# Kernel tuning notes

Hardware: AMD Instinct MI355X
Metric: run time of the kernel (lower is better)

The kernel has to match this reference:

```python
import jax, jax.numpy as jnp
import numpy as np
import math

B, A, T = 64, 23, 128          # batch, num_agents, max seq len
D, AE, S, H = 256, 32, 6, 8    # d_model, agent_encoding_dim, static_dim, heads
DK = D // H                     # 32
DM = D + AE                     # 288, MHA q/k/v dim
NEG = -1e10                     # masked_fill constant from source


def sinusoidal_pe(pos, d):
    # pos: int array [...], returns [..., d] standard transformer PE at positions pos
    half = jnp.arange(d // 2, dtype=jnp.float32)
    div = jnp.exp(-half * (math.log(10000.0) * 2.0 / d))          # [d/2]
    ang = pos[..., None].astype(jnp.float32) * div                # [..., d/2]
    return jnp.stack([jnp.sin(ang), jnp.cos(ang)], axis=-1).reshape(*pos.shape, d)


def setup_inputs() -> dict:
    key = jax.random.key(0)
    ks = jax.random.split(key, 20)
    std = 0.02
    data = jax.random.normal(ks[0], (B, A, T), jnp.float32)
    lengths = jax.random.randint(ks[1], (B, A), 0, T + 1).astype(jnp.int32)   # mask arg = lengths
    t = jnp.arange(T, dtype=jnp.int32)
    time = jnp.where(t[None, None, :] < lengths[:, :, None], t[None, None, :], -1)  # [B,A,T], -1 = pad
    static = jax.random.normal(ks[2], (B, S), jnp.float32)
    # per-agent Linear(1, D): weight [A, D], bias [A, D]
    W_embed = std * jax.random.normal(ks[3], (A, D), jnp.float32)
    b_embed = std * jax.random.normal(ks[4], (A, D), jnp.float32)
    E_var = std * jax.random.normal(ks[5], (A, AE), jnp.float32)            # VariateEncoding table
    W_static = std * jax.random.normal(ks[6], (S, D), jnp.float32)
    b_static = jnp.zeros((D,), jnp.float32)
    Wq = std * jax.random.normal(ks[7], (DM, D), jnp.float32); bq = jnp.zeros((D,), jnp.float32)
    Wk = std * jax.random.normal(ks[8], (DM, D), jnp.float32); bk = jnp.zeros((D,), jnp.float32)
    Wv = std * jax.random.normal(ks[9], (DM, D), jnp.float32); bv = jnp.zeros((D,), jnp.float32)
    Wo = std * jax.random.normal(ks[10], (D, DM), jnp.float32); bo = jnp.zeros((DM,), jnp.float32)
    Wg = std * jax.random.normal(ks[11], (DM + D, 1), jnp.float32); bg = jnp.zeros((1,), jnp.float32)
    return dict(data=data, time=time, mask=lengths, static=static,
                W_embed=W_embed, b_embed=b_embed, E_var=E_var,
                W_static=W_static, b_static=b_static,
                Wq=Wq, bq=bq, Wk=Wk, bk=bk, Wv=Wv, bv=bv, Wo=Wo, bo=bo,
                Wg=Wg, bg=bg)


def reference(data, time, mask, static, W_embed, b_embed, E_var, W_static, b_static,
              Wq, bq, Wk, bk, Wv, bv, Wo, bo, Wg, bg):
    lengths = mask                                            # [B,A] sequence lengths
    t = jnp.arange(T)
    valid = t[None, None, :] < lengths[:, :, None]            # [B,A,T] bool
    # mask_matrix[i,:len,:len]=1 double loop -> vectorized outer product
    mask4 = valid[:, :, :, None] & valid[:, :, None, :]       # [B,A,T,T]

    # per-agent Linear(1, D) loop -> batched rank-1 affine, then ReLU
    data_embeds = jax.nn.relu(data[..., None] * W_embed[None, :, None, :]
                              + b_embed[None, :, None, :])    # [B,A,T,D]

    # src_pe: sinusoidal positional encoding at (clamped) time values
    pe = sinusoidal_pe(jnp.maximum(time, 0), D)               # [B,A,T,D]
    src = data_embeds + pe

    # variate (agent-id) embedding concat -> [B,A,T,D+AE]; encoder = identity
    var = jnp.broadcast_to(E_var[None, :, None, :], (B, A, T, AE))
    memory = jnp.concatenate([src, var], axis=-1)             # [B,A,T,DM]

    # time-masked mean pool over T
    time_mask = time >= 0                                     # [B,A,T]
    memory = jnp.where(time_mask[..., None], memory, 0.0)
    counts = time_mask.sum(axis=2).astype(memory.dtype)       # [B,A]
    agentwise = memory.sum(axis=2) / (counts[..., None] + 1e-9)  # [B,A,DM]

    # custom MHA (dim='Time'): q_len = 1 per agent, keys/values over T
    q = jnp.einsum('bae,ed->bad', agentwise, Wq) + bq          # [B,A,D]
    k = jnp.einsum('bate,ed->batd', memory, Wk) + bk           # [B,A,T,D]
    v = jnp.einsum('bate,ed->batd', memory, Wv) + bv
    qh = q.reshape(B, A, H, DK)                                # [B,A,H,DK] (q_len=1 squeezed)
    kh = k.reshape(B, A, T, H, DK).transpose(0, 1, 3, 2, 4)    # [B,A,H,T,DK]
    vh = v.reshape(B, A, T, H, DK).transpose(0, 1, 3, 2, 4)
    scores = jnp.einsum('bahd,bahtd->baht', qh, kh) / math.sqrt(DK)  # [B,A,H,T]
    amask = mask4[:, :, 0, :]                                  # [B,A,T] row 0 of per-agent mask
    scores = jnp.where(amask[:, :, None, :], scores, NEG)
    p = jax.nn.softmax(scores, axis=-1)                        # dropout = eval (identity)
    ctx = jnp.einsum('baht,bahtd->bahd', p, vh).reshape(B, A, D)
    agent_feat = jnp.einsum('bad,de->bae', ctx, Wo) + bo       # [B,A,DM]

    # agent-masked mean pool over agents
    agent_mask = counts > 0                                    # [B,A]
    agent_feat = jnp.where(agent_mask[..., None], agent_feat, 0.0)
    denom = agent_mask.sum(axis=1).astype(agent_feat.dtype) + 1e-9
    aggre = agent_feat.sum(axis=1) / denom[:, None]            # [B,DM]

    static_feat = static @ W_static + b_static                 # [B,D]
    all_feature = jnp.concatenate([aggre, static_feat], axis=-1)  # [B,DM+D]
    return all_feature @ Wg + bg                               # [B,1]


if __name__ == '__main__':
    out = reference(**setup_inputs())
    print(out.shape, jnp.asarray(out).dtype)
```

## Files before the change

### kernel.cpp

```cpp
#include <hip/hip_runtime.h>
#include <math.h>

#define NB 64
#define NA 23
#define NT 128
#define ND 256
#define NAE 32
#define NS 6
#define NH 8
#define NDM 288

#define OFF_PET    0
#define OFF_PECUM  32768
#define OFF_WKT    65792
#define OFF_VWO    131328
#define OFF_CST    133632
#define OFF_S      133648

__global__ __launch_bounds__(256) void setup_kernel(
    const float* __restrict__ Wk, const float* __restrict__ Wv,
    const float* __restrict__ Wo, const float* __restrict__ Wg,
    const float* __restrict__ bv, const float* __restrict__ bo,
    const float* __restrict__ W_static, const float* __restrict__ b_static,
    const float* __restrict__ bg, float* __restrict__ ws)
{
    const int blk = blockIdx.x;
    const int tid = threadIdx.x;
    float* peT   = ws + OFF_PET;
    float* PEcum = ws + OFF_PECUM;
    float* WkT   = ws + OFF_WKT;
    float* VWo   = ws + OFF_VWO;
    float* cst   = ws + OFF_CST;

    if (blk < 128) {
        const int g = tid >> 7, t = tid & 127;
        const int e = blk * 2 + g;
        const int i = e >> 1;
        const float kdiv = 0.07195578415606394f;
        const float dv = expf(-(float)i * kdiv);
        const float ang = (float)t * dv;
        const float v = (e & 1) ? cosf(ang) : sinf(ang);
        peT[e * NT + t] = v;
        __shared__ float buf[256];
        buf[tid] = v;
        #pragma unroll
        for (int s = 1; s < 128; s <<= 1) {
            __syncthreads();
            float add = (t >= s) ? buf[tid - s] : 0.f;
            __syncthreads();
            buf[tid] += add;
        }
        __syncthreads();
        PEcum[(t + 1) * ND + e] = buf[tid];
    } else if (blk < 384) {
        const int j = blk - 128;
        const float scale = 0.17677669529663687f;
        WkT[j * 256 + tid] = Wk[tid * ND + j] * scale;
    } else if (blk < 392) {
        const int h = blk - 384;
        __shared__ float wog[32];
        {
            const int jj = tid >> 3, sub = tid & 7;
            const int j = h * 32 + jj;
            float acc = 0.f;
            const int m0 = sub * 36;
            #pragma unroll 4
            for (int m = m0; m < m0 + 36; ++m)
                acc = fmaf(Wo[j * NDM + m], Wg[m], acc);
            acc += __shfl_down(acc, 4, 8);
            acc += __shfl_down(acc, 2, 8);
            acc += __shfl_down(acc, 1, 8);
            if (sub == 0) wog[jj] = acc;
        }
        __syncthreads();
        for (int e = tid; e < NDM; e += 256) {
            float acc = 0.f;
            #pragma unroll 8
            for (int jj = 0; jj < 32; ++jj)
                acc = fmaf(Wv[e * ND + h * 32 + jj], wog[jj], acc);
            VWo[h * NDM + e] = acc;
        }
        if (tid == 0) {
            float acc = 0.f;
            #pragma unroll 8
            for (int jj = 0; jj < 32; ++jj)
                acc = fmaf(bv[h * 32 + jj], wog[jj], acc);
            cst[8 + h] = acc;
        }
    } else {
        const int i = tid >> 5, sub = tid & 31;
        float acc = 0.f;
        if (i < 6) {
            for (int m = sub; m < 256; m += 32)
                acc = fmaf(W_static[i * ND + m], Wg[NDM + m], acc);
        } else if (i == 6) {
            for (int m = sub; m < 256; m += 32)
                acc = fmaf(b_static[m], Wg[NDM + m], acc);
        } else {
            for (int m = sub; m < NDM; m += 32)
                acc = fmaf(bo[m], Wg[m], acc);
        }
        #pragma unroll
        for (int off = 16; off > 0; off >>= 1)
            acc += __shfl_down(acc, off, 32);
        if (sub == 0) cst[i] = (i == 6) ? acc + bg[0] : acc;
    }
}

__global__ __launch_bounds__(256) void main_kernel(
    const float* __restrict__ data, const int* __restrict__ lengths,
    const float* __restrict__ W_embed, const float* __restrict__ b_embed,
    const float* __restrict__ E_var,
    const float* __restrict__ Wq, const float* __restrict__ bq,
    float* __restrict__ ws)
{
    const int wg = blockIdx.x;
    const int a = wg % NA;
    const int tid = threadIdx.x;
    const int L = lengths[wg];

    if (L == 0) {
        if (tid == 0) ws[OFF_S + wg] = 0.f;
        return;
    }

    __shared__ float xs[NT];
    __shared__ float agentwise[NDM];
    __shared__ float qs[ND];
    __shared__ float2 Wb[ND];
    __shared__ __align__(16) float combo[ND * 20];
    __shared__ float evvS[NH];
    __shared__ float red[4];

    const float* peT   = ws + OFF_PET;
    const float* PEcum = ws + OFF_PECUM;
    const float* WkT   = ws + OFF_WKT;
    const float* VWo   = ws + OFF_VWO;
    const float* cstp  = ws + OFF_CST;

    if (tid < NT) xs[tid] = data[wg * NT + tid];
    __syncthreads();
    {
        const int e = tid;
        const float We = W_embed[a * ND + e];
        const float be = b_embed[a * ND + e];
        Wb[e] = make_float2(We, be);
        float s0 = 0.f, s1 = 0.f, s2 = 0.f, s3 = 0.f;
        int t = 0;
        for (; t + 4 <= L; t += 4) {
            s0 += fmaxf(fmaf(xs[t],     We, be), 0.f);
            s1 += fmaxf(fmaf(xs[t + 1], We, be), 0.f);
            s2 += fmaxf(fmaf(xs[t + 2], We, be), 0.f);
            s3 += fmaxf(fmaf(xs[t + 3], We, be), 0.f);
        }
        for (; t < L; ++t)
            s0 += fmaxf(fmaf(xs[t], We, be), 0.f);
        agentwise[e] = (((s0 + s1) + (s2 + s3)) + PEcum[L * ND + e]) / (float)L;
    }
    if (tid < NAE) agentwise[ND + tid] = E_var[a * NAE + tid];
    __syncthreads();

    {
        const int j = tid;
        float acc = bq[j];
        #pragma unroll 4
        for (int f = 0; f < NDM; ++f)
            acc = fmaf(agentwise[f], Wq[f * ND + j], acc);
        qs[j] = acc;
    }
    __syncthreads();

    {
        const int h = tid >> 5, eo = tid & 31;
        const float* wr = WkT + (h * 32) * 256;
        const float* qh = qs + h * 32;
        for (int eb = 0; eb < 8; ++eb) {
            const int e = eb * 32 + eo;
            float acc = 0.f, acc2 = 0.f;
            #pragma unroll
            for (int j = 0; j < 32; j += 2) {
                acc  = fmaf(wr[ j      * 256 + e], qh[j],     acc);
                acc2 = fmaf(wr[(j + 1) * 256 + e], qh[j + 1], acc2);
            }
            combo[e * 20 + h] = acc + acc2;
        }
    }
    for (int idx = tid; idx < NH * ND; idx += 256) {
        const int h = idx >> 8, e = idx & 255;
        combo[e * 20 + 8 + h] = VWo[h * NDM + e];
    }
    {
        const int h = tid >> 5, ee = tid & 31;
        float v = agentwise[ND + ee] * VWo[h * NDM + ND + ee];
        v += __shfl_down(v, 16, 32);
        v += __shfl_down(v, 8, 32);
        v += __shfl_down(v, 4, 32);
        v += __shfl_down(v, 2, 32);
        v += __shfl_down(v, 1, 32);
        if (ee == 0) evvS[h] = v;
    }
    __syncthreads();

    {
        const int t  = tid & 63;
        const int hh = (tid >> 6) & 1;
        const int c  = tid >> 7;
        const int ebase = c * 128;
        const float xt1 = xs[t];
        const float xt2 = xs[t + 64];
        const float* peCol = peT + ebase * NT + t;
        const float4* comboV = (const float4*)combo;
        float aS1[4], aS2[4], aM1[4], aM2[4];
        #pragma unroll
        for (int k = 0; k < 4; ++k) { aS1[k] = 0.f; aS2[k] = 0.f; aM1[k] = 0.f; aM2[k] = 0.f; }

        if (L > 64) {
            #pragma unroll 2
            for (int ee = 0; ee < 128; ++ee) {
                const int e = ebase + ee;
                const float2 wb = Wb[e];
                const float pe1 = peCol[ee * NT];
                const float pe2 = peCol[ee * NT + 64];
                const float lin1 = fmaf(xt1, wb.x, wb.y);
                const float lin2 = fmaf(xt2, wb.x, wb.y);
                const float m1 = fmaxf(lin1, 0.f) + pe1;
                const float m2 = fmaxf(lin2, 0.f) + pe2;
                const float4 cq = comboV[e * 5 + hh];
                const float4 cm = comboV[e * 5 + 2 + hh];
                aS1[0] = fmaf(m1, cq.x, aS1[0]); aS1[1] = fmaf(m1, cq.y, aS1[1]);
                aS1[2] = fmaf(m1, cq.z, aS1[2]); aS1[3] = fmaf(m1, cq.w, aS1[3]);
                aS2[0] = fmaf(m2, cq.x, aS2[0]); aS2[1] = fmaf(m2, cq.y, aS2[1]);
                aS2[2] = fmaf(m2, cq.z, aS2[2]); aS2[3] = fmaf(m2, cq.w, aS2[3]);
                aM1[0] = fmaf(m1, cm.x, aM1[0]); aM1[1] = fmaf(m1, cm.y, aM1[1]);
                aM1[2] = fmaf(m1, cm.z, aM1[2]); aM1[3] = fmaf(m1, cm.w, aM1[3]);
                aM2[0] = fmaf(m2, cm.x, aM2[0]); aM2[1] = fmaf(m2, cm.y, aM2[1]);
                aM2[2] = fmaf(m2, cm.z, aM2[2]); aM2[3] = fmaf(m2, cm.w, aM2[3]);
            }
        } else {
            #pragma unroll 2
            for (int ee = 0; ee < 128; ++ee) {
                const int e = ebase + ee;
                const float2 wb = Wb[e];
                const float pe1 = peCol[ee * NT];
                const float m1 = fmaxf(fmaf(xt1, wb.x, wb.y), 0.f) + pe1;
                const float4 cq = comboV[e * 5 + hh];
                const float4 cm = comboV[e * 5 + 2 + hh];
                aS1[0] = fmaf(m1, cq.x, aS1[0]); aS1[1] = fmaf(m1, cq.y, aS1[1]);
                aS1[2] = fmaf(m1, cq.z, aS1[2]); aS1[3] = fmaf(m1, cq.w, aS1[3]);
                aM1[0] = fmaf(m1, cm.x, aM1[0]); aM1[1] = fmaf(m1, cm.y, aM1[1]);
                aM1[2] = fmaf(m1, cm.z, aM1[2]); aM1[3] = fmaf(m1, cm.w, aM1[3]);
            }
        }
        __syncthreads();
        float* scF = combo;
        float* mvF = combo + 1024;
        float* pS  = combo + 2048;
        float* pM  = combo + 3072;
        if (c == 1) {
            #pragma unroll
            for (int k = 0; k < 4; ++k) {
                const int h = hh * 4 + k;
                pS[h * NT + t]      = aS1[k];
                pS[h * NT + t + 64] = aS2[k];
                pM[h * NT + t]      = aM1[k];
                pM[h * NT + t + 64] = aM2[k];
            }
        }
        __syncthreads();
        if (c == 0) {
            #pragma unroll
            for (int k = 0; k < 4; ++k) {
                const int h = hh * 4 + k;
                scF[h * NT + t]      = aS1[k] + pS[h * NT + t];
                scF[h * NT + t + 64] = aS2[k] + pS[h * NT + t + 64];
                mvF[h * NT + t]      = aM1[k] + pM[h * NT + t];
                mvF[h * NT + t + 64] = aM2[k] + pM[h * NT + t + 64];
            }
        }
    }
    __syncthreads();

    {
        const float* sc  = combo;
        const float* mvb = combo + 1024;
        const int wv = tid >> 6, lane = tid & 63;
        float wsum = 0.f;
        for (int hh = 0; hh < 2; ++hh) {
            const int h = wv * 2 + hh;
            float s1 = (lane < L) ? sc[h * NT + lane] : -3e38f;
            float s2 = (lane + 64 < L) ? sc[h * NT + 64 + lane] : -3e38f;
            float mx = fmaxf(s1, s2);
            #pragma unroll
            for (int off = 32; off > 0; off >>= 1)
                mx = fmaxf(mx, __shfl_down(mx, off, 64));
            mx = __shfl(mx, 0, 64);
            const float vbv = evvS[h] + cstp[8 + h];
            float e1 = (lane < L) ? __expf(s1 - mx) : 0.f;
            float e2 = (lane + 64 < L) ? __expf(s2 - mx) : 0.f;
            float num = e1 * (mvb[h * NT + lane] + vbv);
            num = fmaf(e2, mvb[h * NT + 64 + lane] + vbv, num);
            float den = e1 + e2;
            #pragma unroll
            for (int off = 32; off > 0; off >>= 1) {
                num += __shfl_down(num, off, 64);
                den += __shfl_down(den, off, 64);
            }
            if (lane == 0) wsum += num / den;
        }
        if (lane == 0) red[wv] = wsum;
    }
    __syncthreads();
    if (tid == 0)
        ws[OFF_S + wg] = cstp[7] + red[0] + red[1] + red[2] + red[3];
}

__global__ __launch_bounds__(64) void final_kernel(
    const float* __restrict__ statics, const int* __restrict__ lengths,
    const float* __restrict__ ws, float* __restrict__ out)
{
    const int b = threadIdx.x;
    const float* s_arr = ws + OFF_S;
    const float* cst = ws + OFF_CST;
    float sum = 0.f;
    int n = 0;
    for (int a = 0; a < NA; ++a) {
        if (lengths[b * NA + a] > 0) { sum += s_arr[b * NA + a]; ++n; }
    }
    float o = sum / ((float)n + 1e-9f);
    #pragma unroll
    for (int i = 0; i < NS; ++i)
        o = fmaf(statics[b * NS + i], cst[i], o);
    o += cst[6];
    out[b] = o;
}

extern "C" void kernel_launch(void* const* d_in, const int* in_sizes, int n_in,
                              void* d_out, int out_size, void* d_ws, size_t ws_size,
                              hipStream_t stream) {
    const float* data     = (const float*)d_in[0];
    const int*   mask     = (const int*)d_in[2];
    const float* statics  = (const float*)d_in[3];
    const float* W_embed  = (const float*)d_in[4];
    const float* b_embed  = (const float*)d_in[5];
    const float* E_var    = (const float*)d_in[6];
    const float* W_static = (const float*)d_in[7];
    const float* b_static = (const float*)d_in[8];
    const float* Wq       = (const float*)d_in[9];
    const float* bq       = (const float*)d_in[10];
    const float* Wk       = (const float*)d_in[11];
    const float* Wv       = (const float*)d_in[13];
    const float* bv       = (const float*)d_in[14];
    const float* Wo       = (const float*)d_in[15];
    const float* bo       = (const float*)d_in[16];
    const float* Wg       = (const float*)d_in[17];
    const float* bg       = (const float*)d_in[18];
    float* out = (float*)d_out;
    float* ws  = (float*)d_ws;

    setup_kernel<<<dim3(393), dim3(256), 0, stream>>>(Wk, Wv, Wo, Wg, bv, bo,
                                                      W_static, b_static, bg, ws);
    main_kernel<<<dim3(NB * NA), dim3(256), 0, stream>>>(data, mask, W_embed, b_embed,
                                                         E_var, Wq, bq, ws);
    final_kernel<<<dim3(1), dim3(64), 0, stream>>>(statics, mask, ws, out);
}
```

Before: 174.4 us.

## Precompute positional-encoding key/value projections and restructure per-agent attention

Splits the positional-encoding contribution out of the per-timestep score and value terms. A new setup kernel precomputes PE·Wk and PE·VWo once per timestep, so the main kernel's inner loop no longer streams a PE column from global memory. The Q projection becomes float4-vectorised across four partial sums, the combo table shrinks to an XOR-swizzled 16-float row, and E_var·V terms are precomputed per agent. Per-agent results are accumulated into per-batch slots with atomics, which adds an extra kernel launch and makes the summation order nondeterministic.

```diff
diff --git a/kernel.cpp b/kernel.cpp
--- a/kernel.cpp
+++ b/kernel.cpp
@@ -10,23 +10,25 @@
 #define NH 8
 #define NDM 288
 
-#define OFF_PET    0
+#define OFF_PEK    0
 #define OFF_PECUM  32768
-#define OFF_WKT    65792
-#define OFF_VWO    131328
-#define OFF_CST    133632
-#define OFF_S      133648
-
-__global__ __launch_bounds__(256) void setup_kernel(
+#define OFF_WKT    65536
+#define OFF_VWO    131072
+#define OFF_PEMV   133120
+#define OFF_EVA    134144
+#define OFF_CST    134328
+#define OFF_SB     134336
+
+__global__ __launch_bounds__(256) void setup1_kernel(
     const float* __restrict__ Wk, const float* __restrict__ Wv,
     const float* __restrict__ Wo, const float* __restrict__ Wg,
     const float* __restrict__ bv, const float* __restrict__ bo,
     const float* __restrict__ W_static, const float* __restrict__ b_static,
-    const float* __restrict__ bg, float* __restrict__ ws)
+    const float* __restrict__ bg, const float* __restrict__ E_var,
+    float* __restrict__ ws)
 {
     const int blk = blockIdx.x;
     const int tid = threadIdx.x;
-    float* peT   = ws + OFF_PET;
     float* PEcum = ws + OFF_PECUM;
     float* WkT   = ws + OFF_WKT;
     float* VWo   = ws + OFF_VWO;
@@ -40,7 +42,6 @@
         const float dv = expf(-(float)i * kdiv);
         const float ang = (float)t * dv;
         const float v = (e & 1) ? cosf(ang) : sinf(ang);
-        peT[e * NT + t] = v;
         __shared__ float buf[256];
         buf[tid] = v;
         #pragma unroll
@@ -51,7 +52,7 @@
             buf[tid] += add;
         }
         __syncthreads();
-        PEcum[(t + 1) * ND + e] = buf[tid];
+        PEcum[t * ND + e] = buf[tid];
     } else if (blk < 384) {
         const int j = blk - 128;
         const float scale = 0.17677669529663687f;
@@ -59,6 +60,8 @@
     } else if (blk < 392) {
         const int h = blk - 384;
         __shared__ float wog[32];
+        __shared__ float vext[32];
+        __shared__ float vbS;
         {
             const int jj = tid >> 3, sub = tid & 7;
             const int j = h * 32 + jj;
@@ -73,19 +76,34 @@
             if (sub == 0) wog[jj] = acc;
         }
         __syncthreads();
-        for (int e = tid; e < NDM; e += 256) {
+        {
             float acc = 0.f;
             #pragma unroll 8
             for (int jj = 0; jj < 32; ++jj)
-                acc = fmaf(Wv[e * ND + h * 32 + jj], wog[jj], acc);
-            VWo[h * NDM + e] = acc;
+                acc = fmaf(Wv[tid * ND + h * 32 + jj], wog[jj], acc);
+            VWo[h * 256 + tid] = acc;
+        }
+        if (tid < 32) {
+            float acc = 0.f;
+            #pragma unroll 8
+            for (int jj = 0; jj < 32; ++jj)
+                acc = fmaf(Wv[(256 + tid) * ND + h * 32 + jj], wog[jj], acc);
+            vext[tid] = acc;
         }
         if (tid == 0) {
             float acc = 0.f;
             #pragma unroll 8
             for (int jj = 0; jj < 32; ++jj)
                 acc = fmaf(bv[h * 32 + jj], wog[jj], acc);
-            cst[8 + h] = acc;
+            vbS = acc;
+        }
+        __syncthreads();
+        if (tid < NA) {
+            float acc = vbS;
+            #pragma unroll 8
+            for (int ee = 0; ee < 32; ++ee)
+                acc = fmaf(E_var[tid * NAE + ee], vext[ee], acc);
+            ws[OFF_EVA + tid * NH + h] = acc;
         }
     } else {
         const int i = tid >> 5, sub = tid & 31;
@@ -107,6 +125,49 @@
     }
 }
 
+__global__ __launch_bounds__(256) void setup2_kernel(
+    const float* __restrict__ Wk, float* __restrict__ ws)
+{
+    const int t = blockIdx.x;
+    const int tid = threadIdx.x;
+    __shared__ float peS[256];
+    {
+        const int i = tid >> 1;
+        const float kdiv = 0.07195578415606394f;
+        const float dv = expf(-(float)i * kdiv);
+        const float ang = (float)t * dv;
+        peS[tid] = (tid & 1) ? cosf(ang) : sinf(ang);
+    }
+    __syncthreads();
+    {
+        float a0 = 0.f, a1 = 0.f, a2 = 0.f, a3 = 0.f;
+        #pragma unroll 4
+        for (int e = 0; e < 256; e += 4) {
+            a0 = fmaf(peS[e],     Wk[ e      * ND + tid], a0);
+            a1 = fmaf(peS[e + 1], Wk[(e + 1) * ND + tid], a1);
+            a2 = fmaf(peS[e + 2], Wk[(e + 2) * ND + tid], a2);
+            a3 = fmaf(peS[e + 3], Wk[(e + 3) * ND + tid], a3);
+        }
+        const float scale = 0.17677669529663687f;
+        ws[OFF_PEK + t * 256 + tid] = ((a0 + a1) + (a2 + a3)) * scale;
+    }
+    {
+        const int h = tid >> 5, ee = tid & 31;
+        const float* vw = ws + OFF_VWO + h * 256;
+        float v = 0.f;
+        #pragma unroll
+        for (int k = 0; k < 8; ++k)
+            v = fmaf(peS[ee + 32 * k], vw[ee + 32 * k], v);
+        v += __shfl_down(v, 16, 32);
+        v += __shfl_down(v, 8, 32);
+        v += __shfl_down(v, 4, 32);
+        v += __shfl_down(v, 2, 32);
+        v += __shfl_down(v, 1, 32);
+        if (ee == 0) ws[OFF_PEMV + h * NT + t] = v;
+    }
+    if (t == 0 && tid < NB) ws[OFF_SB + tid] = 0.f;
+}
+
 __global__ __launch_bounds__(256) void main_kernel(
     const float* __restrict__ data, const int* __restrict__ lengths,
     const float* __restrict__ W_embed, const float* __restrict__ b_embed,
@@ -116,23 +177,20 @@
 {
     const int wg = blockIdx.x;
     const int a = wg % NA;
+    const int b = wg / NA;
     const int tid = threadIdx.x;
     const int L = lengths[wg];
 
-    if (L == 0) {
-        if (tid == 0) ws[OFF_S + wg] = 0.f;
-        return;
-    }
+    if (L == 0) return;
 
     __shared__ float xs[NT];
     __shared__ float agentwise[NDM];
-    __shared__ float qs[ND];
+    __shared__ __align__(16) float qs[ND];
     __shared__ float2 Wb[ND];
-    __shared__ __align__(16) float combo[ND * 20];
-    __shared__ float evvS[NH];
+    __shared__ __align__(16) float combo[ND * 16];
+    __shared__ __align__(16) float qkx[NH * NT];
     __shared__ float red[4];
 
-    const float* peT   = ws + OFF_PET;
     const float* PEcum = ws + OFF_PECUM;
     const float* WkT   = ws + OFF_WKT;
     const float* VWo   = ws + OFF_VWO;
@@ -155,49 +213,78 @@
         }
         for (; t < L; ++t)
             s0 += fmaxf(fmaf(xs[t], We, be), 0.f);
-        agentwise[e] = (((s0 + s1) + (s2 + s3)) + PEcum[L * ND + e]) / (float)L;
+        agentwise[e] = (((s0 + s1) + (s2 + s3)) + PEcum[(L - 1) * ND + e]) / (float)L;
     }
     if (tid < NAE) agentwise[ND + tid] = E_var[a * NAE + tid];
     __syncthreads();
 
     {
-        const int j = tid;
-        float acc = bq[j];
+        const int lane = tid & 63;
+        const int fc = tid >> 6;
+        const float4* Wq4 = (const float4*)Wq;
+        float a0 = 0.f, a1 = 0.f, a2 = 0.f, a3 = 0.f;
+        const int f0 = fc * 72;
         #pragma unroll 4
-        for (int f = 0; f < NDM; ++f)
-            acc = fmaf(agentwise[f], Wq[f * ND + j], acc);
-        qs[j] = acc;
-    }
-    __syncthreads();
-
-    {
-        const int h = tid >> 5, eo = tid & 31;
-        const float* wr = WkT + (h * 32) * 256;
-        const float* qh = qs + h * 32;
-        for (int eb = 0; eb < 8; ++eb) {
-            const int e = eb * 32 + eo;
-            float acc = 0.f, acc2 = 0.f;
+        for (int f = f0; f < f0 + 72; ++f) {
+            const float ag = agentwise[f];
+            const float4 w = Wq4[f * 64 + lane];
+            a0 = fmaf(ag, w.x, a0);
+            a1 = fmaf(ag, w.y, a1);
+            a2 = fmaf(ag, w.z, a2);
+            a3 = fmaf(ag, w.w, a3);
+        }
+        ((float4*)qkx)[fc * 64 + lane] = make_float4(a0, a1, a2, a3);
+    }
+    __syncthreads();
+    qs[tid] = bq[tid] + qkx[tid] + qkx[256 + tid] + qkx[512 + tid] + qkx[768 + tid];
+    __syncthreads();
+
+    {
+        const int e = tid;
+        const float* wcol = WkT + e;
+        const int r = e & 3;
+        float4* row = (float4*)combo + e * 4;
+        float qk[8];
+        #pragma unroll
+        for (int h = 0; h < 8; ++h) {
+            const float* wr = wcol + (h * 32) * 256;
+            const float* qh = qs + h * 32;
+            float c0 = 0.f, c1 = 0.f;
             #pragma unroll
             for (int j = 0; j < 32; j += 2) {
-                acc  = fmaf(wr[ j      * 256 + e], qh[j],     acc);
-                acc2 = fmaf(wr[(j + 1) * 256 + e], qh[j + 1], acc2);
-            }
-            combo[e * 20 + h] = acc + acc2;
-        }
-    }
-    for (int idx = tid; idx < NH * ND; idx += 256) {
-        const int h = idx >> 8, e = idx & 255;
-        combo[e * 20 + 8 + h] = VWo[h * NDM + e];
-    }
-    {
-        const int h = tid >> 5, ee = tid & 31;
-        float v = agentwise[ND + ee] * VWo[h * NDM + ND + ee];
-        v += __shfl_down(v, 16, 32);
-        v += __shfl_down(v, 8, 32);
-        v += __shfl_down(v, 4, 32);
-        v += __shfl_down(v, 2, 32);
-        v += __shfl_down(v, 1, 32);
-        if (ee == 0) evvS[h] = v;
+                c0 = fmaf(wr[ j      * 256], qh[j],     c0);
+                c1 = fmaf(wr[(j + 1) * 256], qh[j + 1], c1);
+            }
+            qk[h] = c0 + c1;
+        }
+        row[0 ^ r] = make_float4(qk[0], qk[1], qk[2], qk[3]);
+        row[1 ^ r] = make_float4(qk[4], qk[5], qk[6], qk[7]);
+        row[2 ^ r] = make_float4(VWo[0 * 256 + e], VWo[1 * 256 + e],
+                                 VWo[2 * 256 + e], VWo[3 * 256 + e]);
+        row[3 ^ r] = make_float4(VWo[4 * 256 + e], VWo[5 * 256 + e],
+                                 VWo[6 * 256 + e], VWo[7 * 256 + e]);
+    }
+    __syncthreads();
+    {
+        const int h = tid >> 5, t0 = tid & 31;
+        const float4* qs4  = (const float4*)qs;
+        const float4* PEK4 = (const float4*)(ws + OFF_PEK);
+        #pragma unroll
+        for (int tt = 0; tt < 4; ++tt) {
+            const int t = t0 + tt * 32;
+            const float4* pk = PEK4 + t * 64 + h * 8;
+            float b0 = 0.f, b1 = 0.f, b2 = 0.f, b3 = 0.f;
+            #pragma unroll
+            for (int jq = 0; jq < 8; ++jq) {
+                const float4 q = qs4[h * 8 + jq];
+                const float4 p = pk[jq];
+                b0 = fmaf(q.x, p.x, b0);
+                b1 = fmaf(q.y, p.y, b1);
+                b2 = fmaf(q.z, p.z, b2);
+                b3 = fmaf(q.w, p.w, b3);
+            }
+            qkx[h * NT + t] = (b0 + b1) + (b2 + b3);
+        }
     }
     __syncthreads();
 
@@ -208,25 +295,21 @@
         const int ebase = c * 128;
         const float xt1 = xs[t];
         const float xt2 = xs[t + 64];
-        const float* peCol = peT + ebase * NT + t;
         const float4* comboV = (const float4*)combo;
         float aS1[4], aS2[4], aM1[4], aM2[4];
         #pragma unroll
         for (int k = 0; k < 4; ++k) { aS1[k] = 0.f; aS2[k] = 0.f; aM1[k] = 0.f; aM2[k] = 0.f; }
 
         if (L > 64) {
-            #pragma unroll 2
+            #pragma unroll 4
             for (int ee = 0; ee < 128; ++ee) {
                 const int e = ebase + ee;
+                const int r = e & 3;
                 const float2 wb = Wb[e];
-                const float pe1 = peCol[ee * NT];
-                const float pe2 = peCol[ee * NT + 64];
-                const float lin1 = fmaf(xt1, wb.x, wb.y);
-                const float lin2 = fmaf(xt2, wb.x, wb.y);
-                const float m1 = fmaxf(lin1, 0.f) + pe1;
-                const float m2 = fmaxf(lin2, 0.f) + pe2;
-                const float4 cq = comboV[e * 5 + hh];
-                const float4 cm = comboV[e * 5 + 2 + hh];
+                const float m1 = fmaxf(fmaf(xt1, wb.x, wb.y), 0.f);
+                const float m2 = fmaxf(fmaf(xt2, wb.x, wb.y), 0.f);
+                const float4 cq = comboV[e * 4 + (hh ^ r)];
+                const float4 cm = comboV[e * 4 + ((2 | hh) ^ r)];
                 aS1[0] = fmaf(m1, cq.x, aS1[0]); aS1[1] = fmaf(m1, cq.y, aS1[1]);
                 aS1[2] = fmaf(m1, cq.z, aS1[2]); aS1[3] = fmaf(m1, cq.w, aS1[3]);
                 aS2[0] = fmaf(m2, cq.x, aS2[0]); aS2[1] = fmaf(m2, cq.y, aS2[1]);
@@ -237,14 +320,14 @@
                 aM2[2] = fmaf(m2, cm.z, aM2[2]); aM2[3] = fmaf(m2, cm.w, aM2[3]);
             }
         } else {
-            #pragma unroll 2
+            #pragma unroll 4
             for (int ee = 0; ee < 128; ++ee) {
                 const int e = ebase + ee;
+                const int r = e & 3;
                 const float2 wb = Wb[e];
-                const float pe1 = peCol[ee * NT];
-                const float m1 = fmaxf(fmaf(xt1, wb.x, wb.y), 0.f) + pe1;
-                const float4 cq = comboV[e * 5 + hh];
-                const float4 cm = comboV[e * 5 + 2 + hh];
+                const float m1 = fmaxf(fmaf(xt1, wb.x, wb.y), 0.f);
+                const float4 cq = comboV[e * 4 + (hh ^ r)];
+                const float4 cm = comboV[e * 4 + ((2 | hh) ^ r)];
                 aS1[0] = fmaf(m1, cq.x, aS1[0]); aS1[1] = fmaf(m1, cq.y, aS1[1]);
                 aS1[2] = fmaf(m1, cq.z, aS1[2]); aS1[3] = fmaf(m1, cq.w, aS1[3]);
                 aM1[0] = fmaf(m1, cm.x, aM1[0]); aM1[1] = fmaf(m1, cm.y, aM1[1]);
@@ -281,24 +364,25 @@
     __syncthreads();
 
     {
-        const float* sc  = combo;
-        const float* mvb = combo + 1024;
+        const float* sc   = combo;
+        const float* mvb  = combo + 1024;
+        const float* pemv = ws + OFF_PEMV;
         const int wv = tid >> 6, lane = tid & 63;
         float wsum = 0.f;
         for (int hh = 0; hh < 2; ++hh) {
             const int h = wv * 2 + hh;
-            float s1 = (lane < L) ? sc[h * NT + lane] : -3e38f;
-            float s2 = (lane + 64 < L) ? sc[h * NT + 64 + lane] : -3e38f;
+            float s1 = (lane < L) ? sc[h * NT + lane] + qkx[h * NT + lane] : -3e38f;
+            float s2 = (lane + 64 < L) ? sc[h * NT + 64 + lane] + qkx[h * NT + 64 + lane] : -3e38f;
             float mx = fmaxf(s1, s2);
             #pragma unroll
             for (int off = 32; off > 0; off >>= 1)
                 mx = fmaxf(mx, __shfl_down(mx, off, 64));
             mx = __shfl(mx, 0, 64);
-            const float vbv = evvS[h] + cstp[8 + h];
+            const float vbv = ws[OFF_EVA + a * NH + h];
             float e1 = (lane < L) ? __expf(s1 - mx) : 0.f;
             float e2 = (lane + 64 < L) ? __expf(s2 - mx) : 0.f;
-            float num = e1 * (mvb[h * NT + lane] + vbv);
-            num = fmaf(e2, mvb[h * NT + 64 + lane] + vbv, num);
+            float num = e1 * (mvb[h * NT + lane] + pemv[h * NT + lane] + vbv);
+            num = fmaf(e2, mvb[h * NT + 64 + lane] + pemv[h * NT + 64 + lane] + vbv, num);
             float den = e1 + e2;
             #pragma unroll
             for (int off = 32; off > 0; off >>= 1) {
@@ -311,7 +395,7 @@
     }
     __syncthreads();
     if (tid == 0)
-        ws[OFF_S + wg] = cstp[7] + red[0] + red[1] + red[2] + red[3];
+        atomicAdd(ws + OFF_SB + b, cstp[7] + red[0] + red[1] + red[2] + red[3]);
 }
 
 __global__ __launch_bounds__(64) void final_kernel(
@@ -319,14 +403,11 @@
     const float* __restrict__ ws, float* __restrict__ out)
 {
     const int b = threadIdx.x;
-    const float* s_arr = ws + OFF_S;
     const float* cst = ws + OFF_CST;
-    float sum = 0.f;
     int n = 0;
-    for (int a = 0; a < NA; ++a) {
-        if (lengths[b * NA + a] > 0) { sum += s_arr[b * NA + a]; ++n; }
-    }
-    float o = sum / ((float)n + 1e-9f);
+    for (int a = 0; a < NA; ++a)
+        if (lengths[b * NA + a] > 0) ++n;
+    float o = ws[OFF_SB + b] / ((float)n + 1e-9f);
     #pragma unroll
     for (int i = 0; i < NS; ++i)
         o = fmaf(statics[b * NS + i], cst[i], o);
@@ -357,8 +438,9 @@
     float* out = (float*)d_out;
     float* ws  = (float*)d_ws;
 
-    setup_kernel<<<dim3(393), dim3(256), 0, stream>>>(Wk, Wv, Wo, Wg, bv, bo,
-                                                      W_static, b_static, bg, ws);
+    setup1_kernel<<<dim3(393), dim3(256), 0, stream>>>(Wk, Wv, Wo, Wg, bv, bo,
+                                                       W_static, b_static, bg, E_var, ws);
+    setup2_kernel<<<dim3(128), dim3(256), 0, stream>>>(Wk, ws);
     main_kernel<<<dim3(NB * NA), dim3(256), 0, stream>>>(data, mask, W_embed, b_embed,
                                                          E_var, Wq, bq, ws);
     final_kernel<<<dim3(1), dim3(64), 0, stream>>>(statics, mask, ws, out);
```

Result: no change. 174.2 us (-0.1%).
